# Kernel optimization log

Hardware: AMD Instinct MI355X
Metric: run time of the kernel (lower is better)

The kernel has to match this reference:

```python
import jax, jax.numpy as jnp
import numpy as np

BIG = 1e10  # large finite value standing in for +inf in masked mins (grad-safe)


def setup_inputs() -> dict:
    key = jax.random.key(0)
    k1, k2, k3 = jax.random.split(key, 3)
    B, C, N = 16, 3, 4096
    x = jax.random.normal(k1, (B, C, N), dtype=jnp.float32)
    y = jax.random.normal(k2, (B, C, N), dtype=jnp.float32)
    mask = jax.random.randint(k3, (B, N), 0, 2, dtype=jnp.int32)
    return {"x": x, "y": y, "mask": mask}


def reference(x, y, mask):
    # x, y: (B, 3, N); mask: (B, N) with 1 = valid point
    xt = jnp.swapaxes(x, 1, 2)  # (B, N, 3)
    yt = jnp.swapaxes(y, 1, 2)  # (B, N, 3)
    xx = jnp.sum(xt * xt, axis=-1)  # (B, N)
    yy = jnp.sum(yt * yt, axis=-1)  # (B, N)
    # squared pairwise distances, P[b, n, m] = ||x_bn - y_bm||^2
    P = xx[:, :, None] + yy[:, None, :] - 2.0 * jnp.einsum("bnd,bmd->bnm", xt, yt)

    valid = mask.astype(bool)                 # (B, N)
    mf = mask.astype(P.dtype)                 # (B, N)
    cnt = jnp.sum(mf, axis=1)                 # (B,) number of valid points per batch

    # direction 1: for each y-point m, min over valid x-rows n; mean over valid m
    mins1 = jnp.min(jnp.where(valid[:, :, None], P, BIG), axis=1)  # (B, N)
    means1 = jnp.sum(mins1 * mf, axis=1) / cnt                      # (B,)

    # direction 2: for each x-point m, min over valid y-cols n; mean over valid m
    mins2 = jnp.min(jnp.where(valid[:, None, :], P, BIG), axis=2)  # (B, N)
    means2 = jnp.sum(mins2 * mf, axis=1) / cnt                      # (B,)

    return jnp.mean(means1) + jnp.mean(means2)
```

## Files before the change

kernel.cpp:

```cpp
#include <hip/hip_runtime.h>

typedef short bf16x8 __attribute__((ext_vector_type(8)));
typedef float f32x16 __attribute__((ext_vector_type(16)));

#define BIG_F 1e10f
constexpr int B = 16;
constexpr int N = 4096;
constexpr int ROWS  = 128;
constexpr int CHUNK = 512;
constexpr int NRB = N / ROWS;
constexpr int NCH = N / CHUNK;

__device__ __forceinline__ void split(float v, unsigned& h, unsigned& l) {
    unsigned hb = __float_as_uint(v) & 0xFFFF0000u;
    h = hb >> 16;
    float r = v - __uint_as_float(hb);
    l = __float_as_uint(r) >> 16;
}

__device__ __forceinline__ float min3f(float a, float b, float c) {
    return fminf(fminf(a, b), c);
}

__device__ __forceinline__ float vmin16(f32x16 C) {
    float u0 = min3f(C[0], C[1], C[2]);
    float u1 = min3f(C[3], C[4], C[5]);
    float u2 = min3f(C[6], C[7], C[8]);
    float u3 = min3f(C[9], C[10], C[11]);
    float u4 = min3f(C[12], C[13], C[14]);
    return min3f(min3f(u0, u1, u2), fminf(u3, u4), C[15]);
}

__global__ __launch_bounds__(256) void chamfer_mfma(
    const float* __restrict__ x, const float* __restrict__ y,
    const int* __restrict__ mask,
    float* __restrict__ rowpart,
    float* __restrict__ colpart,
    float* __restrict__ out)
{
    const int rb = blockIdx.x;
    const int b  = blockIdx.y;
    const int t  = threadIdx.x;

    __shared__ __align__(16) unsigned short Apack[2][ROWS][8];
    __shared__ __align__(16) unsigned short Bpack[2][CHUNK][8];
    __shared__ float colbuf[8][CHUNK];

    if (rb == 0 && b == 0 && t == 0) out[0] = 0.0f;

    const float* xb = x + (size_t)b * 3 * N;
    const float* yb = y + (size_t)b * 3 * N;
    const int*   mb = mask + b * N;

    if (t < ROWS) {
        int n = rb * ROWS + t;
        float x0 = xb[n], x1 = xb[N + n], x2 = xb[2 * N + n];
        float madd = mb[n] ? 0.0f : BIG_F;
        float xx = fmaf(x2, x2, fmaf(x1, x1, x0 * x0)) + madd;
        unsigned h0, l0, h1, l1, h2, l2, xh, xl;
        split(-2.0f * x0, h0, l0);
        split(-2.0f * x1, h1, l1);
        split(-2.0f * x2, h2, l2);
        split(xx, xh, xl);
        uint4 w0 = { h0 | (h1 << 16), h2 | (h0 << 16), h1 | (h2 << 16), l0 | (l1 << 16) };
        *(uint4*)&Apack[0][t][0] = w0;
        uint4 w1 = { l2 | (l0 << 16), l1 | (l2 << 16), xh | (xl << 16), 0x3F803F80u };
        *(uint4*)&Apack[1][t][0] = w1;
    }

    auto packB = [&](int c, float y0, float y1, float y2, int mval) {
        float madd = mval ? 0.0f : BIG_F;
        float yy = fmaf(y2, y2, fmaf(y1, y1, y0 * y0)) + madd;
        unsigned h0, l0, h1, l1, h2, l2, qh, ql;
        split(y0, h0, l0);
        split(y1, h1, l1);
        split(y2, h2, l2);
        split(yy, qh, ql);
        unsigned u0 = h0 | (h1 << 16);
        unsigned u1 = h2 | (l0 << 16);
        unsigned u2 = l1 | (l2 << 16);
        uint4 w0 = { u0, u1, u2, u0 };
        *(uint4*)&Bpack[0][c][0] = w0;
        uint4 w1 = { u1, u2, 0x3F803F80u, qh | (ql << 16) };
        *(uint4*)&Bpack[1][c][0] = w1;
    };

    float pa0, pa1, pa2, pb0, pb1, pb2; int pam, pbm;
    {
        int m0 = t, m1 = t + 256;
        pa0 = yb[m0]; pa1 = yb[N + m0]; pa2 = yb[2 * N + m0]; pam = mb[m0];
        pb0 = yb[m1]; pb1 = yb[N + m1]; pb2 = yb[2 * N + m1]; pbm = mb[m1];
    }
    packB(t, pa0, pa1, pa2, pam);
    packB(t + 256, pb0, pb1, pb2, pbm);
    {
        int m0 = CHUNK + t, m1 = m0 + 256;
        pa0 = yb[m0]; pa1 = yb[N + m0]; pa2 = yb[2 * N + m0]; pam = mb[m0];
        pb0 = yb[m1]; pb1 = yb[N + m1]; pb2 = yb[2 * N + m1]; pbm = mb[m1];
    }
    __syncthreads();

    const int w    = t >> 6;
    const int L    = t & 63;
    const int half = L >> 5;
    const int lc   = L & 31;

    bf16x8 afr = *(const bf16x8*)&Apack[half][w * 32 + lc][0];
    const unsigned short* Bb = &Bpack[half][lc][0];
    float* cbw = &colbuf[w * 2 + half][lc];

    float rm[16];
#pragma unroll
    for (int r = 0; r < 16; ++r) rm[r] = 1e30f;

    const f32x16 z16 = {0.f,0.f,0.f,0.f,0.f,0.f,0.f,0.f,
                        0.f,0.f,0.f,0.f,0.f,0.f,0.f,0.f};

    for (int ch = 0; ch < NCH; ++ch) {
#pragma unroll
        for (int p = 0; p < 8; ++p) {
            bf16x8 bf0 = *(const bf16x8*)(Bb + p * 512);
            bf16x8 bf1 = *(const bf16x8*)(Bb + p * 512 + 256);
            f32x16 C0 = __builtin_amdgcn_mfma_f32_32x32x16_bf16(afr, bf0, z16, 0, 0, 0);
            f32x16 C1 = __builtin_amdgcn_mfma_f32_32x32x16_bf16(afr, bf1, z16, 0, 0, 0);
#pragma unroll
            for (int r = 0; r < 16; ++r) rm[r] = min3f(rm[r], C0[r], C1[r]);
            cbw[p * 64]      = vmin16(C0);
            cbw[p * 64 + 32] = vmin16(C1);
        }
        __syncthreads();
        float* cpo = colpart + ((size_t)b * NRB + rb) * N + ch * CHUNK;
#pragma unroll
        for (int i = 0; i < 2; ++i) {
            int c = t + i * 256;
            const float* s0 = &colbuf[0][c];
            float v = s0[0];
#pragma unroll
            for (int j = 1; j < 8; ++j) v = fminf(v, s0[j * CHUNK]);
            cpo[c] = v;
        }
        if (ch + 1 < NCH) {
            packB(t, pa0, pa1, pa2, pam);
            packB(t + 256, pb0, pb1, pb2, pbm);
            if (ch + 2 < NCH) {
                int m0 = (ch + 2) * CHUNK + t, m1 = m0 + 256;
                pa0 = yb[m0]; pa1 = yb[N + m0]; pa2 = yb[2 * N + m0]; pam = mb[m0];
                pb0 = yb[m1]; pb1 = yb[N + m1]; pb2 = yb[2 * N + m1]; pbm = mb[m1];
            }
            __syncthreads();
        }
    }

#pragma unroll
    for (int off = 1; off <= 16; off <<= 1)
#pragma unroll
        for (int r = 0; r < 16; ++r)
            rm[r] = fminf(rm[r], __shfl_xor(rm[r], off));
    if (lc == 0) {
        float* rp = rowpart + (size_t)b * N + rb * ROWS + w * 32 + half * 4;
#pragma unroll
        for (int r = 0; r < 16; ++r)
            rp[(r & 3) + 8 * (r >> 2)] = rm[r];
    }
}

__global__ __launch_bounds__(256) void finalize_kernel(
    const int* __restrict__ mask,
    const float* __restrict__ rowpart, const float* __restrict__ colpart,
    float* __restrict__ out)
{
    const int b = blockIdx.x & 15;
    const int q = blockIdx.x >> 4;
    const int t = threadIdx.x;
    const int* mrow = mask + b * N;

    int cnt = 0;
    for (int i = t; i < N / 4; i += 256) {
        int4 mk = ((const int4*)mrow)[i];
        cnt += mk.x + mk.y + mk.z + mk.w;
    }

    const int p0 = q * 1024 + t * 4;
    const float* cp = colpart + (size_t)b * NRB * N + p0;
    float4 mn = *(const float4*)cp;
#pragma unroll 4
    for (int pb = 1; pb < NRB; ++pb) {
        float4 v = *(const float4*)(cp + (size_t)pb * N);
        mn.x = fminf(mn.x, v.x); mn.y = fminf(mn.y, v.y);
        mn.z = fminf(mn.z, v.z); mn.w = fminf(mn.w, v.w);
    }
    float4 rp = *(const float4*)(rowpart + (size_t)b * N + p0);
    int4 mk = *(const int4*)(mrow + p0);
    float s = (mk.x ? (mn.x + rp.x) : 0.f) + (mk.y ? (mn.y + rp.y) : 0.f)
            + (mk.z ? (mn.z + rp.z) : 0.f) + (mk.w ? (mn.w + rp.w) : 0.f);

    for (int off = 32; off > 0; off >>= 1) {
        s   += __shfl_down(s, off);
        cnt += __shfl_down(cnt, off);
    }
    __shared__ float rs[4];
    __shared__ int   rc[4];
    const int wv = t >> 6;
    if ((t & 63) == 0) { rs[wv] = s; rc[wv] = cnt; }
    __syncthreads();
    if (t == 0) {
        float S = rs[0] + rs[1] + rs[2] + rs[3];
        float C = (float)(rc[0] + rc[1] + rc[2] + rc[3]);
        atomicAdd(out, (S / C) * (1.0f / 16.0f));
    }
}

extern "C" void kernel_launch(void* const* d_in, const int* in_sizes, int n_in,
                              void* d_out, int out_size, void* d_ws, size_t ws_size,
                              hipStream_t stream) {
    const float* x    = (const float*)d_in[0];
    const float* y    = (const float*)d_in[1];
    const int*   mask = (const int*)d_in[2];

    float* rowpart = (float*)d_ws;
    float* colpart = rowpart + (size_t)B * N;

    chamfer_mfma<<<dim3(NRB, B), 256, 0, stream>>>(
        x, y, mask, rowpart, colpart, (float*)d_out);
    finalize_kernel<<<dim3(64), 256, 0, stream>>>(
        mask, rowpart, colpart, (float*)d_out);
}
```

Baseline: 102.7 us.

## Split column range across blocks to raise grid parallelism

Each block now handles one 128-row by 512-column tile instead of sweeping all columns, so the grid grows from 32x16 to 256x16 blocks. Row minima become per-column-block partials that the finalize kernel reduces, and the in-loop column reduction uses a cross-half shuffle so colbuf shrinks to four rows. This removes the serial chunk loop, its per-chunk barriers and the register prefetch, aiming to fill the GPU with more blocks. In exchange the A tile is reloaded by every block, rowpart traffic grows eightfold, and finalize does more reduction work.

```diff
diff --git a/kernel.cpp b/kernel.cpp
--- a/kernel.cpp
+++ b/kernel.cpp
@@ -6,10 +6,10 @@
 #define BIG_F 1e10f
 constexpr int B = 16;
 constexpr int N = 4096;
-constexpr int ROWS  = 128;
-constexpr int CHUNK = 512;
+constexpr int ROWS = 128;
+constexpr int COLS = 512;
 constexpr int NRB = N / ROWS;
-constexpr int NCH = N / CHUNK;
+constexpr int NCB = N / COLS;
 
 __device__ __forceinline__ void split(float v, unsigned& h, unsigned& l) {
     unsigned hb = __float_as_uint(v) & 0xFFFF0000u;
@@ -31,22 +31,23 @@
     return min3f(min3f(u0, u1, u2), fminf(u3, u4), C[15]);
 }
 
-__global__ __launch_bounds__(256) void chamfer_mfma(
+__global__ __launch_bounds__(256, 4) void chamfer_mfma(
     const float* __restrict__ x, const float* __restrict__ y,
     const int* __restrict__ mask,
     float* __restrict__ rowpart,
     float* __restrict__ colpart,
     float* __restrict__ out)
 {
-    const int rb = blockIdx.x;
+    const int rb = blockIdx.x & 31;
+    const int cb = blockIdx.x >> 5;
     const int b  = blockIdx.y;
     const int t  = threadIdx.x;
 
     __shared__ __align__(16) unsigned short Apack[2][ROWS][8];
-    __shared__ __align__(16) unsigned short Bpack[2][CHUNK][8];
-    __shared__ float colbuf[8][CHUNK];
-
-    if (rb == 0 && b == 0 && t == 0) out[0] = 0.0f;
+    __shared__ __align__(16) unsigned short Bpack[2][COLS][8];
+    __shared__ float colbuf[4][COLS];
+
+    if (blockIdx.x == 0 && b == 0 && t == 0) out[0] = 0.0f;
 
     const float* xb = x + (size_t)b * 3 * N;
     const float* yb = y + (size_t)b * 3 * N;
@@ -68,8 +69,12 @@
         *(uint4*)&Apack[1][t][0] = w1;
     }
 
-    auto packB = [&](int c, float y0, float y1, float y2, int mval) {
-        float madd = mval ? 0.0f : BIG_F;
+#pragma unroll
+    for (int i = 0; i < 2; ++i) {
+        int c = t + i * 256;
+        int m = cb * COLS + c;
+        float y0 = yb[m], y1 = yb[N + m], y2 = yb[2 * N + m];
+        float madd = mb[m] ? 0.0f : BIG_F;
         float yy = fmaf(y2, y2, fmaf(y1, y1, y0 * y0)) + madd;
         unsigned h0, l0, h1, l1, h2, l2, qh, ql;
         split(y0, h0, l0);
@@ -83,20 +88,6 @@
         *(uint4*)&Bpack[0][c][0] = w0;
         uint4 w1 = { u1, u2, 0x3F803F80u, qh | (ql << 16) };
         *(uint4*)&Bpack[1][c][0] = w1;
-    };
-
-    float pa0, pa1, pa2, pb0, pb1, pb2; int pam, pbm;
-    {
-        int m0 = t, m1 = t + 256;
-        pa0 = yb[m0]; pa1 = yb[N + m0]; pa2 = yb[2 * N + m0]; pam = mb[m0];
-        pb0 = yb[m1]; pb1 = yb[N + m1]; pb2 = yb[2 * N + m1]; pbm = mb[m1];
-    }
-    packB(t, pa0, pa1, pa2, pam);
-    packB(t + 256, pb0, pb1, pb2, pbm);
-    {
-        int m0 = CHUNK + t, m1 = m0 + 256;
-        pa0 = yb[m0]; pa1 = yb[N + m0]; pa2 = yb[2 * N + m0]; pam = mb[m0];
-        pb0 = yb[m1]; pb1 = yb[N + m1]; pb2 = yb[2 * N + m1]; pbm = mb[m1];
     }
     __syncthreads();
 
@@ -107,7 +98,6 @@
 
     bf16x8 afr = *(const bf16x8*)&Apack[half][w * 32 + lc][0];
     const unsigned short* Bb = &Bpack[half][lc][0];
-    float* cbw = &colbuf[w * 2 + half][lc];
 
     float rm[16];
 #pragma unroll
@@ -116,38 +106,20 @@
     const f32x16 z16 = {0.f,0.f,0.f,0.f,0.f,0.f,0.f,0.f,
                         0.f,0.f,0.f,0.f,0.f,0.f,0.f,0.f};
 
-    for (int ch = 0; ch < NCH; ++ch) {
-#pragma unroll
-        for (int p = 0; p < 8; ++p) {
-            bf16x8 bf0 = *(const bf16x8*)(Bb + p * 512);
-            bf16x8 bf1 = *(const bf16x8*)(Bb + p * 512 + 256);
-            f32x16 C0 = __builtin_amdgcn_mfma_f32_32x32x16_bf16(afr, bf0, z16, 0, 0, 0);
-            f32x16 C1 = __builtin_amdgcn_mfma_f32_32x32x16_bf16(afr, bf1, z16, 0, 0, 0);
-#pragma unroll
-            for (int r = 0; r < 16; ++r) rm[r] = min3f(rm[r], C0[r], C1[r]);
-            cbw[p * 64]      = vmin16(C0);
-            cbw[p * 64 + 32] = vmin16(C1);
-        }
-        __syncthreads();
-        float* cpo = colpart + ((size_t)b * NRB + rb) * N + ch * CHUNK;
-#pragma unroll
-        for (int i = 0; i < 2; ++i) {
-            int c = t + i * 256;
-            const float* s0 = &colbuf[0][c];
-            float v = s0[0];
-#pragma unroll
-            for (int j = 1; j < 8; ++j) v = fminf(v, s0[j * CHUNK]);
-            cpo[c] = v;
-        }
-        if (ch + 1 < NCH) {
-            packB(t, pa0, pa1, pa2, pam);
-            packB(t + 256, pb0, pb1, pb2, pbm);
-            if (ch + 2 < NCH) {
-                int m0 = (ch + 2) * CHUNK + t, m1 = m0 + 256;
-                pa0 = yb[m0]; pa1 = yb[N + m0]; pa2 = yb[2 * N + m0]; pam = mb[m0];
-                pb0 = yb[m1]; pb1 = yb[N + m1]; pb2 = yb[2 * N + m1]; pbm = mb[m1];
-            }
-            __syncthreads();
+#pragma unroll
+    for (int p = 0; p < 8; ++p) {
+        bf16x8 bf0 = *(const bf16x8*)(Bb + p * 512);
+        bf16x8 bf1 = *(const bf16x8*)(Bb + p * 512 + 256);
+        f32x16 C0 = __builtin_amdgcn_mfma_f32_32x32x16_bf16(afr, bf0, z16, 0, 0, 0);
+        f32x16 C1 = __builtin_amdgcn_mfma_f32_32x32x16_bf16(afr, bf1, z16, 0, 0, 0);
+#pragma unroll
+        for (int r = 0; r < 16; ++r) rm[r] = min3f(rm[r], C0[r], C1[r]);
+        float v0 = vmin16(C0), v1 = vmin16(C1);
+        v0 = fminf(v0, __shfl_xor(v0, 32));
+        v1 = fminf(v1, __shfl_xor(v1, 32));
+        if (half == 0) {
+            colbuf[w][p * 64 + lc]      = v0;
+            colbuf[w][p * 64 + 32 + lc] = v1;
         }
     }
 
@@ -157,10 +129,20 @@
         for (int r = 0; r < 16; ++r)
             rm[r] = fminf(rm[r], __shfl_xor(rm[r], off));
     if (lc == 0) {
-        float* rp = rowpart + (size_t)b * N + rb * ROWS + w * 32 + half * 4;
+        float* rp = rowpart + ((size_t)b * NCB + cb) * N + rb * ROWS + w * 32 + half * 4;
 #pragma unroll
         for (int r = 0; r < 16; ++r)
             rp[(r & 3) + 8 * (r >> 2)] = rm[r];
+    }
+
+    __syncthreads();
+    float* cpo = colpart + ((size_t)b * NRB + rb) * N + cb * COLS;
+#pragma unroll
+    for (int i = 0; i < 2; ++i) {
+        int c = t + i * 256;
+        float v = fminf(fminf(colbuf[0][c], colbuf[1][c]),
+                        fminf(colbuf[2][c], colbuf[3][c]));
+        cpo[c] = v;
     }
 }
 
@@ -181,6 +163,7 @@
     }
 
     const int p0 = q * 1024 + t * 4;
+
     const float* cp = colpart + (size_t)b * NRB * N + p0;
     float4 mn = *(const float4*)cp;
 #pragma unroll 4
@@ -189,10 +172,17 @@
         mn.x = fminf(mn.x, v.x); mn.y = fminf(mn.y, v.y);
         mn.z = fminf(mn.z, v.z); mn.w = fminf(mn.w, v.w);
     }
-    float4 rp = *(const float4*)(rowpart + (size_t)b * N + p0);
+    const float* rp = rowpart + (size_t)b * NCB * N + p0;
+    float4 rn = *(const float4*)rp;
+#pragma unroll
+    for (int pb = 1; pb < NCB; ++pb) {
+        float4 v = *(const float4*)(rp + (size_t)pb * N);
+        rn.x = fminf(rn.x, v.x); rn.y = fminf(rn.y, v.y);
+        rn.z = fminf(rn.z, v.z); rn.w = fminf(rn.w, v.w);
+    }
     int4 mk = *(const int4*)(mrow + p0);
-    float s = (mk.x ? (mn.x + rp.x) : 0.f) + (mk.y ? (mn.y + rp.y) : 0.f)
-            + (mk.z ? (mn.z + rp.z) : 0.f) + (mk.w ? (mn.w + rp.w) : 0.f);
+    float s = (mk.x ? (mn.x + rn.x) : 0.f) + (mk.y ? (mn.y + rn.y) : 0.f)
+            + (mk.z ? (mn.z + rn.z) : 0.f) + (mk.w ? (mn.w + rn.w) : 0.f);
 
     for (int off = 32; off > 0; off >>= 1) {
         s   += __shfl_down(s, off);
@@ -218,9 +208,9 @@
     const int*   mask = (const int*)d_in[2];
 
     float* rowpart = (float*)d_ws;
-    float* colpart = rowpart + (size_t)B * N;
-
-    chamfer_mfma<<<dim3(NRB, B), 256, 0, stream>>>(
+    float* colpart = rowpart + (size_t)B * NCB * N;
+
+    chamfer_mfma<<<dim3(NRB * NCB, B), 256, 0, stream>>>(
         x, y, mask, rowpart, colpart, (float*)d_out);
     finalize_kernel<<<dim3(64), 256, 0, stream>>>(
         mask, rowpart, colpart, (float*)d_out);
```

New measurement: 306.6 us. +198.6%, slower.
